# Optimization experiments

Hardware: AMD Instinct MI355X
Metric: run time of the kernel (lower is better)

The kernel has to match this reference:

```python
import jax, jax.numpy as jnp
import numpy as np

B, S, D = 8, 2048, 256
H, DFF, L = 8, 1024, 5
DK = D // H
EPS = 1e-5


def _xavier(key, shape):
    fan_in, fan_out = shape[-2], shape[-1]
    a = jnp.sqrt(6.0 / (fan_in + fan_out))
    return jax.random.uniform(key, shape, jnp.float32, -a, a)


def setup_inputs() -> dict:
    key = jax.random.key(0)
    ks = jax.random.split(key, 12)
    inp = {
        "src": jax.random.normal(ks[0], (B, S, D), jnp.float32),
        "sph": jax.random.normal(ks[1], (B, S, S), jnp.float32),
        # stacked per-layer parameters, leading dim = L
        "Wq": _xavier(ks[2], (L, D, D)), "bq": jnp.zeros((L, D), jnp.float32),
        "Wk": _xavier(ks[3], (L, D, D)), "bk": jnp.zeros((L, D), jnp.float32),
        "Wv": _xavier(ks[4], (L, D, D)), "bv": jnp.zeros((L, D), jnp.float32),
        "Wo": _xavier(ks[5], (L, D, D)), "bo": jnp.zeros((L, D), jnp.float32),
        "W1": _xavier(ks[6], (L, D, DFF)), "b1": jnp.zeros((L, DFF), jnp.float32),
        "W2": _xavier(ks[7], (L, DFF, D)), "b2": jnp.zeros((L, D), jnp.float32),
        "ln1_g": jnp.ones((L, D), jnp.float32), "ln1_b": jnp.zeros((L, D), jnp.float32),
        "ln2_g": jnp.ones((L, D), jnp.float32), "ln2_b": jnp.zeros((L, D), jnp.float32),
    }
    return inp


def _layernorm(x, g, b):
    mu = jnp.mean(x, axis=-1, keepdims=True)
    var = jnp.mean(jnp.square(x - mu), axis=-1, keepdims=True)
    return (x - mu) * jax.lax.rsqrt(var + EPS) * g + b


def _layer(x, sph, Wq, bq, Wk, bk, Wv, bv, Wo, bo, W1, b1, W2, b2, g1, be1, g2, be2):
    # multihead attention with additive sph score bias
    q = (x @ Wq + bq).reshape(B, S, H, DK)
    k = (x @ Wk + bk).reshape(B, S, H, DK)
    v = (x @ Wv + bv).reshape(B, S, H, DK)
    scores = jnp.einsum("bqhd,bkhd->bhqk", q, k) / jnp.sqrt(jnp.float32(DK))
    scores = scores + sph[:, None, :, :]  # bias broadcast over heads
    attn = jax.nn.softmax(scores, axis=-1)
    ctx = jnp.einsum("bhqk,bkhd->bqhd", attn, v).reshape(B, S, D)
    src2 = ctx @ Wo + bo
    x = _layernorm(x + src2, g1, be1)
    # FFN (exact gelu, matching torch F.gelu default)
    h = jax.nn.gelu(x @ W1 + b1, approximate=False)
    src2 = h @ W2 + b2
    x = _layernorm(x + src2, g2, be2)
    return x


def reference(src, sph, Wq, bq, Wk, bk, Wv, bv, Wo, bo, W1, b1, W2, b2, ln1_g, ln1_b, ln2_g, ln2_b):
    x = src
    for i in range(L):
        x = _layer(x, sph, Wq[i], bq[i], Wk[i], bk[i], Wv[i], bv[i], Wo[i], bo[i],
                   W1[i], b1[i], W2[i], b2[i], ln1_g[i], ln1_b[i], ln2_g[i], ln2_b[i])
    return x
```

## Files before the change

### kernel.cpp

```cpp
#include <hip/hip_runtime.h>
#include <hip/hip_bf16.h>
#include <cstdint>

__device__ __forceinline__ float b2f(unsigned short u) {
    unsigned int t = ((unsigned int)u) << 16;
    float f;
    __builtin_memcpy(&f, &t, 4);
    return f;
}
__device__ __forceinline__ unsigned short f2b(float f) {
    unsigned int u;
    __builtin_memcpy(&u, &f, 4);
    unsigned int r = (u + 0x7FFFu + ((u >> 16) & 1u)) >> 16;
    return (unsigned short)r;
}
__device__ __forceinline__ unsigned int pkbf(float a, float b) {
    __hip_bfloat162 t = __float22bfloat162_rn(float2{a, b});
    unsigned int u;
    __builtin_memcpy(&u, &t, 4);
    return u;
}
__device__ __forceinline__ float2 bpair(unsigned int u) {
    float2 r;
    unsigned int lo = u << 16;
    unsigned int hi = u & 0xFFFF0000u;
    __builtin_memcpy(&r.x, &lo, 4);
    __builtin_memcpy(&r.y, &hi, 4);
    return r;
}

typedef __attribute__((ext_vector_type(8))) short bf16x8;
typedef __attribute__((ext_vector_type(4))) float f32x4;

#define LOG2E 1.4426950408889634f
#define SC2   0.2550348595f

__device__ __forceinline__ void gload16(const void* g, void* l) {
    __builtin_amdgcn_global_load_lds(
        (const __attribute__((address_space(1))) unsigned int*)g,
        (__attribute__((address_space(3))) unsigned int*)l, 16, 0, 0);
}

__global__ void transcvt_k(const float* __restrict__ in,
                           unsigned short* __restrict__ out, int R, int C,
                           int in_z, int out_z) {
    __shared__ float tile[32][33];
    in += (size_t)blockIdx.z * in_z;
    out += (size_t)blockIdx.z * out_z;
    const int c0 = blockIdx.x * 32, r0 = blockIdx.y * 32;
    const int tx = threadIdx.x, ty = threadIdx.y;
#pragma unroll
    for (int i = 0; i < 32; i += 8)
        tile[ty + i][tx] = in[(size_t)(r0 + ty + i) * C + c0 + tx];
    __syncthreads();
#pragma unroll
    for (int i = 0; i < 32; i += 8)
        out[(size_t)(c0 + ty + i) * R + r0 + tx] = f2b(tile[tx][ty + i]);
}

__global__ __launch_bounds__(256) void sph_cvt(const float* __restrict__ in,
                                               unsigned short* __restrict__ out) {
    const size_t idx = (size_t)blockIdx.x * 256 + threadIdx.x;
    const float4 a = ((const float4*)in)[idx * 2];
    const float4 b = ((const float4*)in)[idx * 2 + 1];
    uint4 o;
    o.x = pkbf(a.x * LOG2E, a.y * LOG2E);
    o.y = pkbf(a.z * LOG2E, a.w * LOG2E);
    o.z = pkbf(b.x * LOG2E, b.y * LOG2E);
    o.w = pkbf(b.z * LOG2E, b.w * LOG2E);
    ((uint4*)out)[idx] = o;
}

__global__ __launch_bounds__(256) void cvt_bf16_k(const float* __restrict__ in,
                                                  unsigned short* __restrict__ out,
                                                  float* __restrict__ xcopy) {
    const size_t idx = (size_t)blockIdx.x * 256 + threadIdx.x;
    const float4 a = ((const float4*)in)[idx * 2];
    const float4 b = ((const float4*)in)[idx * 2 + 1];
    uint4 o;
    o.x = pkbf(a.x, a.y);
    o.y = pkbf(a.z, a.w);
    o.z = pkbf(b.x, b.y);
    o.w = pkbf(b.z, b.w);
    ((uint4*)out)[idx] = o;
    ((float4*)xcopy)[idx * 2] = a;
    ((float4*)xcopy)[idx * 2 + 1] = b;
}

template <int TN, int QKVB>
__global__ __launch_bounds__(256) void gemm_gl_kernel(
    const unsigned short* __restrict__ A, const unsigned short* __restrict__ Wt,
    const float* __restrict__ biasQ, const float* __restrict__ biasK,
    const float* __restrict__ biasV, unsigned short* __restrict__ C,
    int M, int N, int K, int do_gelu) {
    constexpr int JN = TN / 32;
    constexpr int NCH = 16 + TN / 8;
    __shared__ unsigned short As[128 * 64];
    __shared__ unsigned short Bs[TN * 64];
    const int tid = threadIdx.x;
    const int lane = tid & 63, wid = tid >> 6;
    const int m0 = blockIdx.y * 128, n0 = blockIdx.x * TN;
    const int wm = (wid >> 1) * 64, wn = (wid & 1) * (TN / 2);
    const int quad = lane >> 4, mrow = lane & 15;
    const int lrow = lane >> 3, lslot = lane & 7;
    f32x4 acc[4][JN] = {};

    for (int kb = 0; kb < K; kb += 64) {
#pragma unroll
        for (int cc = 0; cc < NCH / 4; ++cc) {
            const int c = wid * (NCH / 4) + cc;
            if (c < 16) {
                const int row = c * 8 + lrow;
                const int gcol = ((lslot ^ (row & 7)) << 3) + kb;
                gload16(A + (size_t)(m0 + row) * K + gcol, &As[c * 512 + lane * 8]);
            } else {
                const int row = (c - 16) * 8 + lrow;
                const int gcol = ((lslot ^ (row & 7)) << 3) + kb;
                gload16(Wt + (size_t)(n0 + row) * K + gcol, &Bs[(c - 16) * 512 + lane * 8]);
            }
        }
        __syncthreads();
#pragma unroll
        for (int h = 0; h < 2; ++h) {
            bf16x8 af[4], bfr[JN];
#pragma unroll
            for (int i = 0; i < 4; i++) {
                const int ar = wm + i * 16 + mrow;
                af[i] = *(const bf16x8*)&As[ar * 64 + (((h * 4 + quad) ^ (ar & 7)) << 3)];
            }
#pragma unroll
            for (int j = 0; j < JN; j++) {
                const int br = wn + j * 16 + mrow;
                bfr[j] = *(const bf16x8*)&Bs[br * 64 + (((h * 4 + quad) ^ (br & 7)) << 3)];
            }
#pragma unroll
            for (int i = 0; i < 4; i++)
#pragma unroll
                for (int j = 0; j < JN; j++)
                    acc[i][j] = __builtin_amdgcn_mfma_f32_16x16x32_bf16(af[i], bfr[j], acc[i][j], 0, 0, 0);
        }
        __syncthreads();
    }

    const float* bp;
    if (QKVB) {
        const int bsel = n0 >> 8;
        bp = bsel == 0 ? biasQ : (bsel == 1 ? biasK : biasV);
    } else {
        bp = biasQ;
    }
#pragma unroll
    for (int i = 0; i < 4; i++)
#pragma unroll
        for (int j = 0; j < JN; j++) {
            const int col = n0 + wn + j * 16 + mrow;
            const float bv = QKVB ? bp[col & 255] : bp[col];
#pragma unroll
            for (int r = 0; r < 4; r++) {
                const int row = m0 + wm + i * 16 + quad * 4 + r;
                float v = acc[i][j][r] + bv;
                if (do_gelu) v = 0.5f * v * (1.0f + erff(v * 0.70710678118654752f));
                C[(size_t)row * N + col] = f2b(v);
            }
        }
}

template <int SPHB16>
__global__ __launch_bounds__(256) void attn_mfma(
    const unsigned short* __restrict__ Qb, const unsigned short* __restrict__ Kb,
    const unsigned short* __restrict__ Vb, const float* __restrict__ sphf,
    const unsigned short* __restrict__ sphb, unsigned short* __restrict__ Ctx) {
    __shared__ unsigned short Ks[64 * 40];
    __shared__ unsigned short Vt[32 * 72];
    __shared__ unsigned short Ps[4][16 * 72];

    const int tid = threadIdx.x, lane = tid & 63, wid = tid >> 6;
    const int quad = lane >> 4, lq = lane & 15;
    const int bid0 = blockIdx.x;
    const int bid = (bid0 & 7) * 256 + (bid0 >> 3);
    const int h = bid >> 8, b = (bid >> 5) & 7, qt = bid & 31;
    const int q0 = qt * 64;
    const size_t bS = (size_t)b * 2048;

    const int skey = tid >> 2, sdg = (tid & 3) << 3;
    const unsigned short* kp = Kb + (bS + skey) * 768 + h * 32 + sdg;
    const int vkp = tid & 31, vdg = (tid >> 5) << 2;
    const int vm = vkp & 15, vc = vkp >> 4;
    const int vso = 2 * vm + 32 * vc;
    const unsigned short* vp = Vb + (bS + vm + 32 * vc) * 768 + h * 32 + vdg;

    const bf16x8 qf = *(const bf16x8*)(Qb + (bS + q0 + wid * 16 + lq) * 768 + h * 32 + quad * 8);

    const size_t sprow = ((size_t)b * 2048 + q0 + wid * 16 + quad * 4) * 2048 + lq;
    const float* spf = sphf + sprow;
    const unsigned short* spb = sphb + sprow;

    float l_r[4] = {0.f, 0.f, 0.f, 0.f};
    f32x4 o0 = {}, o1 = {};

    for (int kt = 0; kt < 32; ++kt) {
        __syncthreads();
        *(uint4*)&Ks[skey * 40 + sdg] = *(const uint4*)kp;
        {
            uint2 va  = *(const uint2*)vp;
            uint2 vb2 = *(const uint2*)(vp + 16 * 768);
            *(unsigned int*)&Vt[(vdg + 0) * 72 + vso] = (va.x & 0xFFFFu) | (vb2.x << 16);
            *(unsigned int*)&Vt[(vdg + 1) * 72 + vso] = (va.x >> 16) | (vb2.x & 0xFFFF0000u);
            *(unsigned int*)&Vt[(vdg + 2) * 72 + vso] = (va.y & 0xFFFFu) | (vb2.y << 16);
            *(unsigned int*)&Vt[(vdg + 3) * 72 + vso] = (va.y >> 16) | (vb2.y & 0xFFFF0000u);
        }
        kp += 64 * 768;
        vp += 64 * 768;
        __syncthreads();

        const f32x4 zf = {};
        __builtin_amdgcn_s_setprio(1);
        f32x4 sa0 = __builtin_amdgcn_mfma_f32_16x16x32_bf16(
            qf, *(const bf16x8*)&Ks[(0  + lq) * 40 + quad * 8], zf, 0, 0, 0);
        f32x4 sa1 = __builtin_amdgcn_mfma_f32_16x16x32_bf16(
            qf, *(const bf16x8*)&Ks[(16 + lq) * 40 + quad * 8], zf, 0, 0, 0);
        f32x4 sa2 = __builtin_amdgcn_mfma_f32_16x16x32_bf16(
            qf, *(const bf16x8*)&Ks[(32 + lq) * 40 + quad * 8], zf, 0, 0, 0);
        f32x4 sa3 = __builtin_amdgcn_mfma_f32_16x16x32_bf16(
            qf, *(const bf16x8*)&Ks[(48 + lq) * 40 + quad * 8], zf, 0, 0, 0);
        __builtin_amdgcn_s_setprio(0);

        const int k0 = kt * 64;
#pragma unroll
        for (int r = 0; r < 4; ++r) {
            float sb0, sb1, sb2, sb3;
            if (SPHB16) {
                const unsigned short* spr = spb + (size_t)r * 2048 + k0;
                sb0 = b2f(spr[0]);  sb1 = b2f(spr[16]);
                sb2 = b2f(spr[32]); sb3 = b2f(spr[48]);
            } else {
                const float* spr = spf + (size_t)r * 2048 + k0;
                sb0 = spr[0]  * LOG2E; sb1 = spr[16] * LOG2E;
                sb2 = spr[32] * LOG2E; sb3 = spr[48] * LOG2E;
            }
            const float p0 = __builtin_amdgcn_exp2f(fmaf(sa0[r], SC2, sb0));
            const float p1 = __builtin_amdgcn_exp2f(fmaf(sa1[r], SC2, sb1));
            const float p2 = __builtin_amdgcn_exp2f(fmaf(sa2[r], SC2, sb2));
            const float p3 = __builtin_amdgcn_exp2f(fmaf(sa3[r], SC2, sb3));
            l_r[r] += (p0 + p1) + (p2 + p3);
            unsigned int* pw = (unsigned int*)&Ps[wid][(quad * 4 + r) * 72];
            pw[lq]      = pkbf(p0, p1);
            pw[lq + 16] = pkbf(p2, p3);
        }

        __builtin_amdgcn_s_setprio(1);
#pragma unroll
        for (int k2 = 0; k2 < 2; ++k2) {
            bf16x8 pf = *(const bf16x8*)&Ps[wid][lq * 72 + k2 * 32 + quad * 8];
            o0 = __builtin_amdgcn_mfma_f32_16x16x32_bf16(
                pf, *(const bf16x8*)&Vt[(0  + lq) * 72 + k2 * 32 + quad * 8], o0, 0, 0, 0);
            o1 = __builtin_amdgcn_mfma_f32_16x16x32_bf16(
                pf, *(const bf16x8*)&Vt[(16 + lq) * 72 + k2 * 32 + quad * 8], o1, 0, 0, 0);
        }
        __builtin_amdgcn_s_setprio(0);
    }

    unsigned short* op = Ctx + (bS + q0 + wid * 16 + quad * 4) * 256 + h * 32;
#pragma unroll
    for (int r = 0; r < 4; ++r) {
        float l = l_r[r];
        l += __shfl_xor(l, 1);
        l += __shfl_xor(l, 2);
        l += __shfl_xor(l, 4);
        l += __shfl_xor(l, 8);
        const float inv = 1.f / l;
        op[r * 256 + lq]      = f2b(o0[r] * inv);
        op[r * 256 + 16 + lq] = f2b(o1[r] * inv);
    }
}

__global__ __launch_bounds__(256) void add_ln_kernel(
    const float* x, const unsigned short* r,
    const float* __restrict__ g, const float* __restrict__ be,
    float* out, unsigned short* xb) {
    const int lane = threadIdx.x & 63, wid = threadIdx.x >> 6;
    const size_t row = (size_t)blockIdx.x * 4 + wid;
    float4 xv = *(const float4*)(x + row * 256 + lane * 4);
    uint2 ru = *(const uint2*)(r + row * 256 + lane * 4);
    float2 ra = bpair(ru.x), rb = bpair(ru.y);
    float v[4] = {xv.x + ra.x, xv.y + ra.y, xv.z + rb.x, xv.w + rb.y};
    float sum = v[0] + v[1] + v[2] + v[3];
#pragma unroll
    for (int off = 32; off; off >>= 1) sum += __shfl_xor(sum, off);
    const float mu = sum * (1.f / 256.f);
    float sq = 0.f;
#pragma unroll
    for (int i = 0; i < 4; i++) { float d = v[i] - mu; sq += d * d; }
#pragma unroll
    for (int off = 32; off; off >>= 1) sq += __shfl_xor(sq, off);
    const float rs = rsqrtf(sq * (1.f / 256.f) + 1e-5f);
    float4 o;
    o.x = (v[0] - mu) * rs * g[lane * 4 + 0] + be[lane * 4 + 0];
    o.y = (v[1] - mu) * rs * g[lane * 4 + 1] + be[lane * 4 + 1];
    o.z = (v[2] - mu) * rs * g[lane * 4 + 2] + be[lane * 4 + 2];
    o.w = (v[3] - mu) * rs * g[lane * 4 + 3] + be[lane * 4 + 3];
    *(float4*)(out + row * 256 + lane * 4) = o;
    uint2 p;
    p.x = pkbf(o.x, o.y);
    p.y = pkbf(o.z, o.w);
    *(uint2*)(xb + row * 256 + lane * 4) = p;
}

extern "C" void kernel_launch(void* const* d_in, const int* in_sizes, int n_in,
                              void* d_out, int out_size, void* d_ws, size_t ws_size,
                              hipStream_t stream) {
    const float* src = (const float*)d_in[0];
    const float* sph = (const float*)d_in[1];
    const float* Wq  = (const float*)d_in[2];
    const float* bq  = (const float*)d_in[3];
    const float* Wk  = (const float*)d_in[4];
    const float* bk  = (const float*)d_in[5];
    const float* Wv  = (const float*)d_in[6];
    const float* bv  = (const float*)d_in[7];
    const float* Wo  = (const float*)d_in[8];
    const float* bo  = (const float*)d_in[9];
    const float* W1  = (const float*)d_in[10];
    const float* b1  = (const float*)d_in[11];
    const float* W2  = (const float*)d_in[12];
    const float* b2  = (const float*)d_in[13];
    const float* g1  = (const float*)d_in[14];
    const float* be1 = (const float*)d_in[15];
    const float* g2  = (const float*)d_in[16];
    const float* be2 = (const float*)d_in[17];

    char* ws = (char*)d_ws;
    float* X = (float*)d_out;
    unsigned short* QKV = (unsigned short*)(ws + 0);
    unsigned short* CTX = (unsigned short*)(ws + 25165824);
    unsigned short* T2  = (unsigned short*)(ws + 33554432);
    unsigned short* H   = QKV;
    unsigned short* XB  = T2;
    unsigned short* WtQKV = (unsigned short*)(ws + 41943040);
    unsigned short* WtO   = (unsigned short*)(ws + 43909120);
    unsigned short* Wt1   = (unsigned short*)(ws + 44564480);
    unsigned short* Wt2   = (unsigned short*)(ws + 47185920);
    unsigned short* SPHB  = (unsigned short*)(ws + 50331648);
    const int use_b16 = (ws_size >= (size_t)117440512);

    const dim3 tb(32, 8);
    transcvt_k<<<dim3(8, 8, 5),  tb, 0, stream>>>(Wq, WtQKV,          256, 256, 65536, 196608);
    transcvt_k<<<dim3(8, 8, 5),  tb, 0, stream>>>(Wk, WtQKV + 65536,  256, 256, 65536, 196608);
    transcvt_k<<<dim3(8, 8, 5),  tb, 0, stream>>>(Wv, WtQKV + 131072, 256, 256, 65536, 196608);
    transcvt_k<<<dim3(8, 8, 5),  tb, 0, stream>>>(Wo, WtO,            256, 256, 65536, 65536);
    transcvt_k<<<dim3(32, 8, 5), tb, 0, stream>>>(W1, Wt1,            256, 1024, 262144, 262144);
    transcvt_k<<<dim3(8, 32, 5), tb, 0, stream>>>(W2, Wt2,            1024, 256, 262144, 262144);
    if (use_b16) sph_cvt<<<16384, 256, 0, stream>>>(sph, SPHB);
    cvt_bf16_k<<<2048, 256, 0, stream>>>(src, XB, X);

    const int M = 16384;
    for (int lyr = 0; lyr < 5; ++lyr) {
        gemm_gl_kernel<128, 1><<<dim3(6, 128), 256, 0, stream>>>(
            XB, WtQKV + lyr * 196608, bq + lyr * 256, bk + lyr * 256, bv + lyr * 256,
            QKV, M, 768, 256, 0);
        if (use_b16)
            attn_mfma<1><<<2048, 256, 0, stream>>>(QKV, QKV + 256, QKV + 512, sph, SPHB, CTX);
        else
            attn_mfma<0><<<2048, 256, 0, stream>>>(QKV, QKV + 256, QKV + 512, sph, SPHB, CTX);
        gemm_gl_kernel<64, 0><<<dim3(4, 128), 256, 0, stream>>>(
            CTX, WtO + lyr * 65536, bo + lyr * 256, nullptr, nullptr, T2, M, 256, 256, 0);
        add_ln_kernel<<<4096, 256, 0, stream>>>(X, T2, g1 + lyr * 256, be1 + lyr * 256, X, XB);
        gemm_gl_kernel<128, 0><<<dim3(8, 128), 256, 0, stream>>>(
            XB, Wt1 + lyr * 262144, b1 + lyr * 1024, nullptr, nullptr, H, M, 1024, 256, 1);
        gemm_gl_kernel<64, 0><<<dim3(4, 128), 256, 0, stream>>>(
            H, Wt2 + lyr * 262144, b2 + lyr * 256, nullptr, nullptr, T2, M, 256, 1024, 0);
        add_ln_kernel<<<4096, 256, 0, stream>>>(X, T2, g2 + lyr * 256, be2 + lyr * 256, X, XB);
    }
}
```

Baseline: 1.436 ms.

## Double-buffer K/V tiles in attention and permute bf16 sph bias layout

The attention kernel now double-buffers its K and V shared-memory tiles. The next tile's global loads are issued into registers before the barrier, which removes one __syncthreads per iteration and overlaps the load latency with MFMA work. The bf16 sph conversion writes a permuted layout so that each lane reads its four bias values with a single 8-byte load instead of four scalar loads. The block-index swizzle is also removed, which changes the order in which heads and batches are scheduled and may affect L2 reuse of the sph rows. Shared-memory use grows, which could reduce occupancy.

```diff
diff --git a/kernel.cpp b/kernel.cpp
--- a/kernel.cpp
+++ b/kernel.cpp
@@ -58,17 +58,24 @@
         out[(size_t)(c0 + ty + i) * R + r0 + tx] = f2b(tile[tx][ty + i]);
 }
 
-__global__ __launch_bounds__(256) void sph_cvt(const float* __restrict__ in,
-                                               unsigned short* __restrict__ out) {
-    const size_t idx = (size_t)blockIdx.x * 256 + threadIdx.x;
-    const float4 a = ((const float4*)in)[idx * 2];
-    const float4 b = ((const float4*)in)[idx * 2 + 1];
-    uint4 o;
-    o.x = pkbf(a.x * LOG2E, a.y * LOG2E);
-    o.y = pkbf(a.z * LOG2E, a.w * LOG2E);
-    o.z = pkbf(b.x * LOG2E, b.y * LOG2E);
-    o.w = pkbf(b.z * LOG2E, b.w * LOG2E);
-    ((uint4*)out)[idx] = o;
+__global__ __launch_bounds__(256) void sph_cvt_perm(const float* __restrict__ in,
+                                                    unsigned short* __restrict__ out) {
+    const int t = threadIdx.x & 127;
+    const size_t row = (size_t)blockIdx.x * 2 + (threadIdx.x >> 7);
+    const int g = t >> 2, q = t & 3;
+    const float* ip = in + row * 2048 + 64 * g + 4 * q;
+    float4 f0 = *(const float4*)(ip);
+    float4 f1 = *(const float4*)(ip + 16);
+    float4 f2 = *(const float4*)(ip + 32);
+    float4 f3 = *(const float4*)(ip + 48);
+    uint4 o0, o1;
+    o0.x = pkbf(f0.x * LOG2E, f1.x * LOG2E); o0.y = pkbf(f2.x * LOG2E, f3.x * LOG2E);
+    o0.z = pkbf(f0.y * LOG2E, f1.y * LOG2E); o0.w = pkbf(f2.y * LOG2E, f3.y * LOG2E);
+    o1.x = pkbf(f0.z * LOG2E, f1.z * LOG2E); o1.y = pkbf(f2.z * LOG2E, f3.z * LOG2E);
+    o1.z = pkbf(f0.w * LOG2E, f1.w * LOG2E); o1.w = pkbf(f2.w * LOG2E, f3.w * LOG2E);
+    unsigned short* op = out + row * 2048 + 64 * g + 16 * q;
+    ((uint4*)op)[0] = o0;
+    ((uint4*)op)[1] = o1;
 }
 
 __global__ __launch_bounds__(256) void cvt_bf16_k(const float* __restrict__ in,
@@ -170,14 +177,13 @@
     const unsigned short* __restrict__ Qb, const unsigned short* __restrict__ Kb,
     const unsigned short* __restrict__ Vb, const float* __restrict__ sphf,
     const unsigned short* __restrict__ sphb, unsigned short* __restrict__ Ctx) {
-    __shared__ unsigned short Ks[64 * 40];
-    __shared__ unsigned short Vt[32 * 72];
+    __shared__ unsigned short Ks[2 * 64 * 40];
+    __shared__ unsigned short Vt[2 * 32 * 72];
     __shared__ unsigned short Ps[4][16 * 72];
 
     const int tid = threadIdx.x, lane = tid & 63, wid = tid >> 6;
     const int quad = lane >> 4, lq = lane & 15;
-    const int bid0 = blockIdx.x;
-    const int bid = (bid0 & 7) * 256 + (bid0 >> 3);
+    const int bid = blockIdx.x;
     const int h = bid >> 8, b = (bid >> 5) & 7, qt = bid & 31;
     const int q0 = qt * 64;
     const size_t bS = (size_t)b * 2048;
@@ -191,38 +197,48 @@
 
     const bf16x8 qf = *(const bf16x8*)(Qb + (bS + q0 + wid * 16 + lq) * 768 + h * 32 + quad * 8);
 
-    const size_t sprow = ((size_t)b * 2048 + q0 + wid * 16 + quad * 4) * 2048 + lq;
-    const float* spf = sphf + sprow;
-    const unsigned short* spb = sphb + sprow;
+    const size_t sprow = ((size_t)b * 2048 + q0 + wid * 16 + quad * 4) * 2048;
+    const float* spf = sphf + sprow + lq;
+    const unsigned short* spb = sphb + sprow + 4 * lq;
 
     float l_r[4] = {0.f, 0.f, 0.f, 0.f};
     f32x4 o0 = {}, o1 = {};
 
+    uint4 kw = *(const uint4*)kp;
+    uint2 va = *(const uint2*)vp;
+    uint2 vb2 = *(const uint2*)(vp + 16 * 768);
+    int c = 0;
+
     for (int kt = 0; kt < 32; ++kt) {
+        *(uint4*)&Ks[c * 2560 + skey * 40 + sdg] = kw;
+        {
+            unsigned short* vt = &Vt[c * 2304];
+            *(unsigned int*)&vt[(vdg + 0) * 72 + vso] = (va.x & 0xFFFFu) | (vb2.x << 16);
+            *(unsigned int*)&vt[(vdg + 1) * 72 + vso] = (va.x >> 16) | (vb2.x & 0xFFFF0000u);
+            *(unsigned int*)&vt[(vdg + 2) * 72 + vso] = (va.y & 0xFFFFu) | (vb2.y << 16);
+            *(unsigned int*)&vt[(vdg + 3) * 72 + vso] = (va.y >> 16) | (vb2.y & 0xFFFF0000u);
+        }
+        if (kt < 31) {
+            kp += 64 * 768;
+            vp += 64 * 768;
+            kw = *(const uint4*)kp;
+            va = *(const uint2*)vp;
+            vb2 = *(const uint2*)(vp + 16 * 768);
+        }
         __syncthreads();
-        *(uint4*)&Ks[skey * 40 + sdg] = *(const uint4*)kp;
-        {
-            uint2 va  = *(const uint2*)vp;
-            uint2 vb2 = *(const uint2*)(vp + 16 * 768);
-            *(unsigned int*)&Vt[(vdg + 0) * 72 + vso] = (va.x & 0xFFFFu) | (vb2.x << 16);
-            *(unsigned int*)&Vt[(vdg + 1) * 72 + vso] = (va.x >> 16) | (vb2.x & 0xFFFF0000u);
-            *(unsigned int*)&Vt[(vdg + 2) * 72 + vso] = (va.y & 0xFFFFu) | (vb2.y << 16);
-            *(unsigned int*)&Vt[(vdg + 3) * 72 + vso] = (va.y >> 16) | (vb2.y & 0xFFFF0000u);
-        }
-        kp += 64 * 768;
-        vp += 64 * 768;
-        __syncthreads();
-
+
+        const unsigned short* ks = &Ks[c * 2560];
+        const unsigned short* vt = &Vt[c * 2304];
         const f32x4 zf = {};
         __builtin_amdgcn_s_setprio(1);
         f32x4 sa0 = __builtin_amdgcn_mfma_f32_16x16x32_bf16(
-            qf, *(const bf16x8*)&Ks[(0  + lq) * 40 + quad * 8], zf, 0, 0, 0);
+            qf, *(const bf16x8*)&ks[(0  + lq) * 40 + quad * 8], zf, 0, 0, 0);
         f32x4 sa1 = __builtin_amdgcn_mfma_f32_16x16x32_bf16(
-            qf, *(const bf16x8*)&Ks[(16 + lq) * 40 + quad * 8], zf, 0, 0, 0);
+            qf, *(const bf16x8*)&ks[(16 + lq) * 40 + quad * 8], zf, 0, 0, 0);
         f32x4 sa2 = __builtin_amdgcn_mfma_f32_16x16x32_bf16(
-            qf, *(const bf16x8*)&Ks[(32 + lq) * 40 + quad * 8], zf, 0, 0, 0);
+            qf, *(const bf16x8*)&ks[(32 + lq) * 40 + quad * 8], zf, 0, 0, 0);
         f32x4 sa3 = __builtin_amdgcn_mfma_f32_16x16x32_bf16(
-            qf, *(const bf16x8*)&Ks[(48 + lq) * 40 + quad * 8], zf, 0, 0, 0);
+            qf, *(const bf16x8*)&ks[(48 + lq) * 40 + quad * 8], zf, 0, 0, 0);
         __builtin_amdgcn_s_setprio(0);
 
         const int k0 = kt * 64;
@@ -230,9 +246,9 @@
         for (int r = 0; r < 4; ++r) {
             float sb0, sb1, sb2, sb3;
             if (SPHB16) {
-                const unsigned short* spr = spb + (size_t)r * 2048 + k0;
-                sb0 = b2f(spr[0]);  sb1 = b2f(spr[16]);
-                sb2 = b2f(spr[32]); sb3 = b2f(spr[48]);
+                const uint2 su = *(const uint2*)(spb + (size_t)r * 2048 + k0);
+                const float2 slo = bpair(su.x), shi = bpair(su.y);
+                sb0 = slo.x; sb1 = slo.y; sb2 = shi.x; sb3 = shi.y;
             } else {
                 const float* spr = spf + (size_t)r * 2048 + k0;
                 sb0 = spr[0]  * LOG2E; sb1 = spr[16] * LOG2E;
@@ -253,11 +269,12 @@
         for (int k2 = 0; k2 < 2; ++k2) {
             bf16x8 pf = *(const bf16x8*)&Ps[wid][lq * 72 + k2 * 32 + quad * 8];
             o0 = __builtin_amdgcn_mfma_f32_16x16x32_bf16(
-                pf, *(const bf16x8*)&Vt[(0  + lq) * 72 + k2 * 32 + quad * 8], o0, 0, 0, 0);
+                pf, *(const bf16x8*)&vt[(0  + lq) * 72 + k2 * 32 + quad * 8], o0, 0, 0, 0);
             o1 = __builtin_amdgcn_mfma_f32_16x16x32_bf16(
-                pf, *(const bf16x8*)&Vt[(16 + lq) * 72 + k2 * 32 + quad * 8], o1, 0, 0, 0);
+                pf, *(const bf16x8*)&vt[(16 + lq) * 72 + k2 * 32 + quad * 8], o1, 0, 0, 0);
         }
         __builtin_amdgcn_s_setprio(0);
+        c ^= 1;
     }
 
     unsigned short* op = Ctx + (bS + q0 + wid * 16 + quad * 4) * 256 + h * 32;
@@ -349,7 +366,7 @@
     transcvt_k<<<dim3(8, 8, 5),  tb, 0, stream>>>(Wo, WtO,            256, 256, 65536, 65536);
     transcvt_k<<<dim3(32, 8, 5), tb, 0, stream>>>(W1, Wt1,            256, 1024, 262144, 262144);
     transcvt_k<<<dim3(8, 32, 5), tb, 0, stream>>>(W2, Wt2,            1024, 256, 262144, 262144);
-    if (use_b16) sph_cvt<<<16384, 256, 0, stream>>>(sph, SPHB);
+    if (use_b16) sph_cvt_perm<<<8192, 256, 0, stream>>>(sph, SPHB);
     cvt_bf16_k<<<2048, 256, 0, stream>>>(src, XB, X);
 
     const int M = 16384;
```

After: 1.410 ms. Within noise of the previous version (-1.8%).
